# Performance work log

Measured on AMD Instinct MI355X. Metric: run time of the kernel, lower is better.

The kernel has to match this reference:

```python
import jax, jax.numpy as jnp
import numpy as np

K = 1024
H = 16
HEAD = K // H

def setup_inputs() -> dict:
    key = jax.random.key(0)
    ks = jax.random.split(key, 6)
    b, t = 2, 2048
    x = jax.random.normal(ks[0], (b, t, K), dtype=jnp.float32)
    padding = jnp.ones((b, t), dtype=jnp.int32)
    s = 1.0 / np.sqrt(K)
    Wq = jax.random.normal(ks[1], (K, K), dtype=jnp.float32) * s
    Wk = jax.random.normal(ks[2], (K, K), dtype=jnp.float32) * s
    Wv = jax.random.normal(ks[3], (K, K), dtype=jnp.float32) * s
    Wo = jax.random.normal(ks[4], (K, K), dtype=jnp.float32) * s
    bo = jnp.zeros((K,), dtype=jnp.float32)
    return {"x": x, "padding": padding, "Wq": Wq, "Wk": Wk, "Wv": Wv, "Wo": Wo, "bo": bo}

def reference(x, padding, Wq, Wk, Wv, Wo, bo):
    b, t, k = x.shape
    h, d = H, HEAD
    # projections (nn.Linear: x @ W.T), then split heads -> [b,h,t,d]
    q = (x @ Wq.T).reshape(b, t, h, d).transpose(0, 2, 1, 3)
    kk = (x @ Wk.T).reshape(b, t, h, d).transpose(0, 2, 1, 3)
    v = (x @ Wv.T).reshape(b, t, h, d).transpose(0, 2, 1, 3)
    scores = jnp.einsum('bhqd,bhkd->bhqk', q, kk)
    # key-side padding mask: positions with padding==0 get -inf (before scaling,
    # same result since -inf/sqrt(d) == -inf)
    mask = (padding == 0)[:, None, None, :]  # [b,1,1,t]
    scores = jnp.where(mask, -jnp.inf, scores) / np.sqrt(d).astype(np.float32)
    weights = jax.nn.softmax(scores, axis=-1)
    out = jnp.einsum('bhqk,bhkd->bhqd', weights, v)
    out = out.transpose(0, 2, 1, 3).reshape(b, t, h * d)
    return out @ Wo.T + bo
```

## Files before the change

### kernel.cpp

```cpp
#include <hip/hip_runtime.h>
#include <hip/hip_bf16.h>
#include <cmath>
#include <stdint.h>

#define K_DIM 1024
#define NH    16
#define HD    64
#define T     2048
#define NTOK  4096
#define NBH   32

typedef __bf16 bf16x8 __attribute__((ext_vector_type(8)));
typedef float  f32x4  __attribute__((ext_vector_type(4)));
typedef float  f32x16 __attribute__((ext_vector_type(16)));

__device__ __forceinline__ unsigned short f2bf(float f) {
  union { float f; unsigned u; } v; v.f = f;
  unsigned u = v.u;
  return (unsigned short)((u + 0x7FFFu + ((u >> 16) & 1u)) >> 16);
}
__device__ __forceinline__ ushort4 pk4(float a, float b, float c, float d) {
  union { __hip_bfloat162 h[2]; ushort4 u; } r;
  r.h[0] = __float22bfloat162_rn(float2{a, b});
  r.h[1] = __float22bfloat162_rn(float2{c, d});
  return r.u;
}
__device__ __forceinline__ int pk2(float a, float b) {
  union { __hip_bfloat162 h; int u; } r;
  r.h = __float22bfloat162_rn(float2{a, b});
  return r.u;
}

__device__ __forceinline__ void gload16(const void* g, void* l) {
  __builtin_amdgcn_global_load_lds(
      (__attribute__((address_space(1))) void*)(g),
      (__attribute__((address_space(3))) void*)(l),
      16, 0, 0);
}

__global__ void convert_kernel(const float* __restrict__ x,
                               const float* __restrict__ Wq,
                               const float* __restrict__ Wk,
                               const float* __restrict__ Wv,
                               const float* __restrict__ Wo,
                               unsigned short* __restrict__ xb,
                               unsigned short* __restrict__ wqkv,
                               unsigned short* __restrict__ wob)
{
  const size_t NX = (size_t)NTOK * K_DIM;
  const size_t NW = (size_t)K_DIM * K_DIM;
  size_t i = ((size_t)blockIdx.x * blockDim.x + threadIdx.x) * 4;
  const float* src; unsigned short* dst; size_t off;
  float scale = 1.f;
  if (i < NX)             { src = x;  dst = xb;          off = i; }
  else if (i < NX + NW)   { src = Wq; dst = wqkv;        off = i - NX;
                            scale = 0.18033688011112042f; }
  else if (i < NX + 2*NW) { src = Wk; dst = wqkv + NW;   off = i - NX - NW; }
  else if (i < NX + 3*NW) { src = Wv; dst = wqkv + 2*NW; off = i - NX - 2*NW; }
  else                    { src = Wo; dst = wob;         off = i - NX - 3*NW; }
  float4 v = *(const float4*)(src + off);
  *(ushort4*)(dst + off) = pk4(v.x * scale, v.y * scale, v.z * scale, v.w * scale);
}

template <int MODE, int TM, int TN>
__global__ __launch_bounds__(256, 2)
void gemm_bt(const unsigned short* __restrict__ A,
             const unsigned short* __restrict__ B,
             unsigned short* __restrict__ o_q,
             unsigned short* __restrict__ o_k,
             unsigned short* __restrict__ o_v,
             float* __restrict__ o_f,
             const float* __restrict__ bias)
{
  __shared__ unsigned short Asm[TM * 64];
  __shared__ unsigned short Bsm[TN * 64];
  const int tid  = threadIdx.x;
  const int wave = tid >> 6;
  const int lane = tid & 63;
  const int lq   = lane & 15;
  const int quad = lane >> 4;
  const int bm = blockIdx.x, bn = blockIdx.y;
  const int wm = (wave >> 1) * (TM / 2), wn = (wave & 1) * (TN / 2);
  const int MT = TM / 32, NT = TN / 32;

  f32x4 acc[MT][NT];
#pragma unroll
  for (int i = 0; i < MT; ++i)
#pragma unroll
    for (int j = 0; j < NT; ++j) acc[i][j] = (f32x4){0.f, 0.f, 0.f, 0.f};

  const char* Ab = (const char*)(A + (size_t)bm * TM * K_DIM);
  const char* Bb = (const char*)(B + (size_t)bn * TN * K_DIM);

  for (int k0 = 0; k0 < K_DIM; k0 += 64) {
#pragma unroll
    for (int i = 0; i < MT; ++i) {
      int off   = i * 4096 + wave * 1024 + lane * 16;
      int row   = off >> 7;
      int chunk = (off >> 4) & 7;
      int scol  = (chunk ^ (row & 7)) << 4;
      gload16(Ab + (size_t)row * (K_DIM * 2) + (size_t)k0 * 2 + scol,
              (char*)Asm + off - lane * 16);
    }
#pragma unroll
    for (int i = 0; i < NT; ++i) {
      int off   = i * 4096 + wave * 1024 + lane * 16;
      int row   = off >> 7;
      int chunk = (off >> 4) & 7;
      int scol  = (chunk ^ (row & 7)) << 4;
      gload16(Bb + (size_t)row * (K_DIM * 2) + (size_t)k0 * 2 + scol,
              (char*)Bsm + off - lane * 16);
    }
    __syncthreads();
#pragma unroll
    for (int kk = 0; kk < 64; kk += 32) {
      bf16x8 af[MT], bfr[NT];
#pragma unroll
      for (int mt = 0; mt < MT; ++mt) {
        int row = wm + mt * 16 + lq;
        int sw  = (quad + (kk >> 3)) ^ (row & 7);
        af[mt] = *(const bf16x8*)((const char*)Asm + row * 128 + (sw << 4));
      }
#pragma unroll
      for (int nt = 0; nt < NT; ++nt) {
        int row = wn + nt * 16 + lq;
        int sw  = (quad + (kk >> 3)) ^ (row & 7);
        bfr[nt] = *(const bf16x8*)((const char*)Bsm + row * 128 + (sw << 4));
      }
#pragma unroll
      for (int mt = 0; mt < MT; ++mt)
#pragma unroll
        for (int nt = 0; nt < NT; ++nt)
          acc[mt][nt] = __builtin_amdgcn_mfma_f32_16x16x32_bf16(af[mt], bfr[nt], acc[mt][nt], 0, 0, 0);
    }
    __syncthreads();
  }

#pragma unroll
  for (int mt = 0; mt < MT; ++mt) {
    int mbase = bm * TM + wm + mt * 16 + quad * 4;
#pragma unroll
    for (int nt = 0; nt < NT; ++nt) {
      int n = bn * TN + wn + nt * 16 + lq;
      if (MODE == 1) {
        int which = mbase >> 10, c = mbase & 1023;
        int h = c >> 6, d0 = c & 63;
        int b = n >> 11, t = n & 2047;
        if (which < 2) {
          ushort4 pk = pk4(acc[mt][nt][0], acc[mt][nt][1], acc[mt][nt][2], acc[mt][nt][3]);
          unsigned short* dst = which ? o_k : o_q;
          *(ushort4*)&dst[((size_t)(b * NH + h) * T + t) * HD + d0] = pk;
        } else {
#pragma unroll
          for (int r = 0; r < 4; ++r)
            o_v[((size_t)(b * NH + h) * HD + d0 + r) * T + t] = f2bf(acc[mt][nt][r]);
        }
      } else {
        float4 bv = *(const float4*)&bias[mbase];
        float4 o;
        o.x = acc[mt][nt][0] + bv.x; o.y = acc[mt][nt][1] + bv.y;
        o.z = acc[mt][nt][2] + bv.z; o.w = acc[mt][nt][3] + bv.w;
        *(float4*)&o_f[(size_t)n * K_DIM + mbase] = o;
      }
    }
  }
}

__global__ __launch_bounds__(256, 2)
void attn_kernel(const unsigned short* __restrict__ Q,
                 const unsigned short* __restrict__ Kb,
                 const unsigned short* __restrict__ Vt,
                 const int* __restrict__ padding,
                 unsigned short* __restrict__ O)
{
  __shared__ unsigned short Ksm[128 * 64];
  __shared__ unsigned short Vsm[2][64 * 128];
  __shared__ float Lsm[4][32];

  const int tid  = threadIdx.x;
  const int wave = tid >> 6;
  const int lane = tid & 63;
  const int l31  = lane & 31;
  const int hw   = lane >> 5;
  const int bh = blockIdx.x;
  const int qt = blockIdx.y;
  const int b  = bh >> 4;
  const int h  = bh & 15;
  const int qbase = qt * 128 + wave * 32;

  bf16x8 qf[4];
#pragma unroll
  for (int kk = 0; kk < 4; ++kk)
    qf[kk] = *(const bf16x8*)&Q[((size_t)bh * T + qbase + l31) * HD + kk * 16 + hw * 8];

  f32x16 o_acc[2];
#pragma unroll
  for (int db = 0; db < 2; ++db)
#pragma unroll
    for (int r = 0; r < 16; ++r) o_acc[db][r] = 0.f;
  float l_part = 0.f;

  auto stage = [&](int kt, int buf) {
#pragma unroll
    for (int i = 0; i < 4; ++i) {
      int off = i * 4096 + wave * 1024 + lane * 16;
      {
        int row = off >> 7, chunk = (off >> 4) & 7;
        int scol = (chunk ^ (row & 7)) << 4;
        gload16((const char*)Kb + ((size_t)(bh * T + kt * 128 + row) * HD) * 2 + scol,
                (char*)Ksm + off - lane * 16);
      }
      {
        int row = off >> 8, chunk = (off >> 4) & 15;
        int scol = (chunk ^ (row & 15)) << 4;
        gload16((const char*)Vt + ((size_t)(bh * HD + row) * T + (size_t)kt * 128) * 2 + scol,
                (char*)Vsm[buf] + off - lane * 16);
      }
    }
  };

  stage(0, 0);
  __syncthreads();

  for (int kt = 0; kt < T / 128; ++kt) {
    const int cur = kt & 1;

    f32x16 st[4];
#pragma unroll
    for (int nt = 0; nt < 4; ++nt)
#pragma unroll
      for (int r = 0; r < 16; ++r) st[nt][r] = 0.f;
#pragma unroll
    for (int kk = 0; kk < 4; ++kk) {
#pragma unroll
      for (int nt = 0; nt < 4; ++nt) {
        int row = nt * 32 + l31;
        int sw  = (2 * kk + hw) ^ (row & 7);
        bf16x8 kf = *(const bf16x8*)((const char*)Ksm + row * 128 + (sw << 4));
        st[nt] = __builtin_amdgcn_mfma_f32_32x32x16_bf16(kf, qf[kk], st[nt], 0, 0, 0);
      }
    }

    __syncthreads();

    if (kt < T / 128 - 1) stage(kt + 1, cur ^ 1);

#pragma unroll
    for (int nt = 0; nt < 4; ++nt) {
      int dw[8];
#pragma unroll
      for (int g = 0; g < 4; ++g) {
        int4 pd = *(const int4*)&padding[b * T + kt * 128 + nt * 32 + g * 8 + hw * 4];
        float p0 = pd.x ? __builtin_amdgcn_exp2f(st[nt][g * 4 + 0]) : 0.f;
        float p1 = pd.y ? __builtin_amdgcn_exp2f(st[nt][g * 4 + 1]) : 0.f;
        float p2 = pd.z ? __builtin_amdgcn_exp2f(st[nt][g * 4 + 2]) : 0.f;
        float p3 = pd.w ? __builtin_amdgcn_exp2f(st[nt][g * 4 + 3]) : 0.f;
        l_part += (p0 + p1) + (p2 + p3);
        dw[g * 2]     = pk2(p0, p1);
        dw[g * 2 + 1] = pk2(p2, p3);
      }
      union PA { int d[4]; bf16x8 v; } pa0, pa1;
      {
        int a0 = dw[0], c0 = dw[2];
        int a1 = dw[1], c1 = dw[3];
        asm("v_permlane32_swap_b32 %0, %1" : "+v"(a0), "+v"(c0));
        asm("v_permlane32_swap_b32 %0, %1" : "+v"(a1), "+v"(c1));
        pa0.d[0] = a0; pa0.d[1] = a1; pa0.d[2] = c0; pa0.d[3] = c1;
        int b0 = dw[4], d0 = dw[6];
        int b1 = dw[5], d1 = dw[7];
        asm("v_permlane32_swap_b32 %0, %1" : "+v"(b0), "+v"(d0));
        asm("v_permlane32_swap_b32 %0, %1" : "+v"(b1), "+v"(d1));
        pa1.d[0] = b0; pa1.d[1] = b1; pa1.d[2] = d0; pa1.d[3] = d1;
      }
#pragma unroll
      for (int j = 0; j < 2; ++j) {
        bf16x8 pav = j ? pa1.v : pa0.v;
#pragma unroll
        for (int db = 0; db < 2; ++db) {
          int row = db * 32 + l31;
          int g2  = 4 * nt + 2 * j + hw;
          int sw  = g2 ^ (row & 15);
          bf16x8 vf = *(const bf16x8*)((const char*)Vsm[cur] + row * 256 + (sw << 4));
          o_acc[db] = __builtin_amdgcn_mfma_f32_32x32x16_bf16(pav, vf, o_acc[db], 0, 0, 0);
        }
      }
    }

    __syncthreads();
  }

  float lsum = l_part + __shfl_xor(l_part, 32);
  float inv  = (lsum > 0.f) ? 1.f / lsum : 0.f;
  Lsm[wave][l31] = inv;
  __syncthreads();
  f32x4 inv4[4];
#pragma unroll
  for (int g = 0; g < 4; ++g)
    inv4[g] = *(const f32x4*)&Lsm[wave][g * 8 + hw * 4];
#pragma unroll
  for (int db = 0; db < 2; ++db) {
#pragma unroll
    for (int r = 0; r < 16; ++r) {
      int qrow = (r & 3) + 8 * (r >> 2) + 4 * hw;
      int t    = qbase + qrow;
      int chan = h * HD + db * 32 + l31;
      O[((size_t)(b * T + t)) * K_DIM + chan] = f2bf(o_acc[db][r] * inv4[r >> 2][r & 3]);
    }
  }
}

extern "C" void kernel_launch(void* const* d_in, const int* in_sizes, int n_in,
                              void* d_out, int out_size, void* d_ws, size_t ws_size,
                              hipStream_t stream)
{
  const float* x       = (const float*)d_in[0];
  const int*   padding = (const int*)d_in[1];
  const float* Wq      = (const float*)d_in[2];
  const float* Wk      = (const float*)d_in[3];
  const float* Wv      = (const float*)d_in[4];
  const float* Wo      = (const float*)d_in[5];
  const float* bo      = (const float*)d_in[6];
  float* out = (float*)d_out;

  char* ws = (char*)d_ws;
  unsigned short* xb   = (unsigned short*)(ws);
  unsigned short* wqkv = (unsigned short*)(ws + (8u  << 20));
  unsigned short* wob  = (unsigned short*)(ws + (14u << 20));
  unsigned short* qb   = (unsigned short*)(ws + (16u << 20));
  unsigned short* kb   = (unsigned short*)(ws + (24u << 20));
  unsigned short* vtb  = (unsigned short*)(ws + (32u << 20));
  unsigned short* ab   = (unsigned short*)(ws + (40u << 20));

  convert_kernel<<<8192, 256, 0, stream>>>(x, Wq, Wk, Wv, Wo, xb, wqkv, wob);

  gemm_bt<1, 192, 128><<<dim3(16, 32), 256, 0, stream>>>(wqkv, xb, qb, kb, vtb, nullptr, nullptr);

  attn_kernel<<<dim3(32, 16), 256, 0, stream>>>(qb, kb, vtb, padding, ab);

  gemm_bt<2, 64, 128><<<dim3(16, 32), 256, 0, stream>>>(wob, ab, nullptr, nullptr, nullptr, out, bo);
}
```

Before: 205.0 us.

## Double-buffer K tiles, prefetch early, interleave QK^T with softmax per tile

K shared-memory staging becomes double-buffered, so the next tile's K and V loads are issued at the start of each iteration rather than after the QK^T pass and a mid-loop barrier. The score computation is restructured to run one 32-key subtile at a time, feeding its exp/PV work directly. This lowers live score registers from four accumulators to one and removes a __syncthreads. The K swizzle also changes to a row-dependent XOR pattern to cut LDS bank conflicts, at the cost of more LDS use, which may affect occupancy at 2 blocks per CU.

```diff
diff --git a/kernel.cpp b/kernel.cpp
--- a/kernel.cpp
+++ b/kernel.cpp
@@ -173,7 +173,7 @@
                  const int* __restrict__ padding,
                  unsigned short* __restrict__ O)
 {
-  __shared__ unsigned short Ksm[128 * 64];
+  __shared__ unsigned short Ksm[2][128 * 64];
   __shared__ unsigned short Vsm[2][64 * 128];
   __shared__ float Lsm[4][32];
 
@@ -187,6 +187,7 @@
   const int b  = bh >> 4;
   const int h  = bh & 15;
   const int qbase = qt * 128 + wave * 32;
+  const int fk   = (l31 & 7) ^ ((l31 >> 3) & 3);
 
   bf16x8 qf[4];
 #pragma unroll
@@ -206,9 +207,10 @@
       int off = i * 4096 + wave * 1024 + lane * 16;
       {
         int row = off >> 7, chunk = (off >> 4) & 7;
-        int scol = (chunk ^ (row & 7)) << 4;
+        int f   = (row & 7) ^ ((row >> 3) & 3);
+        int scol = (chunk ^ f) << 4;
         gload16((const char*)Kb + ((size_t)(bh * T + kt * 128 + row) * HD) * 2 + scol,
-                (char*)Ksm + off - lane * 16);
+                (char*)Ksm[buf] + off - lane * 16);
       }
       {
         int row = off >> 8, chunk = (off >> 4) & 15;
@@ -225,36 +227,29 @@
   for (int kt = 0; kt < T / 128; ++kt) {
     const int cur = kt & 1;
 
-    f32x16 st[4];
-#pragma unroll
-    for (int nt = 0; nt < 4; ++nt)
-#pragma unroll
-      for (int r = 0; r < 16; ++r) st[nt][r] = 0.f;
-#pragma unroll
-    for (int kk = 0; kk < 4; ++kk) {
-#pragma unroll
-      for (int nt = 0; nt < 4; ++nt) {
+    if (kt < T / 128 - 1) stage(kt + 1, cur ^ 1);
+
+#pragma unroll
+    for (int nt = 0; nt < 4; ++nt) {
+      f32x16 st;
+#pragma unroll
+      for (int r = 0; r < 16; ++r) st[r] = 0.f;
+#pragma unroll
+      for (int kk = 0; kk < 4; ++kk) {
         int row = nt * 32 + l31;
-        int sw  = (2 * kk + hw) ^ (row & 7);
-        bf16x8 kf = *(const bf16x8*)((const char*)Ksm + row * 128 + (sw << 4));
-        st[nt] = __builtin_amdgcn_mfma_f32_32x32x16_bf16(kf, qf[kk], st[nt], 0, 0, 0);
-      }
-    }
-
-    __syncthreads();
-
-    if (kt < T / 128 - 1) stage(kt + 1, cur ^ 1);
-
-#pragma unroll
-    for (int nt = 0; nt < 4; ++nt) {
+        int sw  = (2 * kk + hw) ^ fk;
+        bf16x8 kf = *(const bf16x8*)((const char*)Ksm[cur] + row * 128 + (sw << 4));
+        st = __builtin_amdgcn_mfma_f32_32x32x16_bf16(kf, qf[kk], st, 0, 0, 0);
+      }
+
       int dw[8];
 #pragma unroll
       for (int g = 0; g < 4; ++g) {
         int4 pd = *(const int4*)&padding[b * T + kt * 128 + nt * 32 + g * 8 + hw * 4];
-        float p0 = pd.x ? __builtin_amdgcn_exp2f(st[nt][g * 4 + 0]) : 0.f;
-        float p1 = pd.y ? __builtin_amdgcn_exp2f(st[nt][g * 4 + 1]) : 0.f;
-        float p2 = pd.z ? __builtin_amdgcn_exp2f(st[nt][g * 4 + 2]) : 0.f;
-        float p3 = pd.w ? __builtin_amdgcn_exp2f(st[nt][g * 4 + 3]) : 0.f;
+        float p0 = pd.x ? __builtin_amdgcn_exp2f(st[g * 4 + 0]) : 0.f;
+        float p1 = pd.y ? __builtin_amdgcn_exp2f(st[g * 4 + 1]) : 0.f;
+        float p2 = pd.z ? __builtin_amdgcn_exp2f(st[g * 4 + 2]) : 0.f;
+        float p3 = pd.w ? __builtin_amdgcn_exp2f(st[g * 4 + 3]) : 0.f;
         l_part += (p0 + p1) + (p2 + p3);
         dw[g * 2]     = pk2(p0, p1);
         dw[g * 2 + 1] = pk2(p2, p3);
```

New measurement: 189.5 us. 1.08x faster.

## Double-buffer K tiles, drop mid-loop barrier, split PV accumulators

Applied to the files above, without the earlier changes.

K shared memory becomes double-buffered, so the next K/V tile can be prefetched at the top of each iteration and the barrier between QK^T and PV is removed. The K swizzle adds a row>>3 term to reduce LDS bank conflicts, and its XOR index is hoisted out of the inner loop. P fragments are built for all tiles before the PV MFMAs, which accumulate into two independent chains that are summed at the end, along with two partial row sums. This costs more LDS (which may limit occupancy with 2 blocks per CU) and more accumulator registers.

```diff
diff --git a/kernel.cpp b/kernel.cpp
--- a/kernel.cpp
+++ b/kernel.cpp
@@ -173,7 +173,7 @@
                  const int* __restrict__ padding,
                  unsigned short* __restrict__ O)
 {
-  __shared__ unsigned short Ksm[128 * 64];
+  __shared__ unsigned short Ksm[2][128 * 64];
   __shared__ unsigned short Vsm[2][64 * 128];
   __shared__ float Lsm[4][32];
 
@@ -187,18 +187,21 @@
   const int b  = bh >> 4;
   const int h  = bh & 15;
   const int qbase = qt * 128 + wave * 32;
+  const int fk   = (l31 & 7) ^ ((l31 >> 3) & 3);
 
   bf16x8 qf[4];
 #pragma unroll
   for (int kk = 0; kk < 4; ++kk)
     qf[kk] = *(const bf16x8*)&Q[((size_t)bh * T + qbase + l31) * HD + kk * 16 + hw * 8];
 
-  f32x16 o_acc[2];
-#pragma unroll
-  for (int db = 0; db < 2; ++db)
-#pragma unroll
-    for (int r = 0; r < 16; ++r) o_acc[db][r] = 0.f;
-  float l_part = 0.f;
+  f32x16 oj[2][2];
+#pragma unroll
+  for (int j = 0; j < 2; ++j)
+#pragma unroll
+    for (int db = 0; db < 2; ++db)
+#pragma unroll
+      for (int r = 0; r < 16; ++r) oj[j][db][r] = 0.f;
+  float lp0 = 0.f, lp1 = 0.f;
 
   auto stage = [&](int kt, int buf) {
 #pragma unroll
@@ -206,9 +209,10 @@
       int off = i * 4096 + wave * 1024 + lane * 16;
       {
         int row = off >> 7, chunk = (off >> 4) & 7;
-        int scol = (chunk ^ (row & 7)) << 4;
+        int f   = (row & 7) ^ ((row >> 3) & 3);
+        int scol = (chunk ^ f) << 4;
         gload16((const char*)Kb + ((size_t)(bh * T + kt * 128 + row) * HD) * 2 + scol,
-                (char*)Ksm + off - lane * 16);
+                (char*)Ksm[buf] + off - lane * 16);
       }
       {
         int row = off >> 8, chunk = (off >> 4) & 15;
@@ -225,6 +229,8 @@
   for (int kt = 0; kt < T / 128; ++kt) {
     const int cur = kt & 1;
 
+    if (kt < T / 128 - 1) stage(kt + 1, cur ^ 1);
+
     f32x16 st[4];
 #pragma unroll
     for (int nt = 0; nt < 4; ++nt)
@@ -232,19 +238,16 @@
       for (int r = 0; r < 16; ++r) st[nt][r] = 0.f;
 #pragma unroll
     for (int kk = 0; kk < 4; ++kk) {
+      int sw = (2 * kk + hw) ^ fk;
 #pragma unroll
       for (int nt = 0; nt < 4; ++nt) {
         int row = nt * 32 + l31;
-        int sw  = (2 * kk + hw) ^ (row & 7);
-        bf16x8 kf = *(const bf16x8*)((const char*)Ksm + row * 128 + (sw << 4));
+        bf16x8 kf = *(const bf16x8*)((const char*)Ksm[cur] + row * 128 + (sw << 4));
         st[nt] = __builtin_amdgcn_mfma_f32_32x32x16_bf16(kf, qf[kk], st[nt], 0, 0, 0);
       }
     }
 
-    __syncthreads();
-
-    if (kt < T / 128 - 1) stage(kt + 1, cur ^ 1);
-
+    union PA { int d[4]; bf16x8 v; } paA[4], paB[4];
 #pragma unroll
     for (int nt = 0; nt < 4; ++nt) {
       int dw[8];
@@ -255,33 +258,37 @@
         float p1 = pd.y ? __builtin_amdgcn_exp2f(st[nt][g * 4 + 1]) : 0.f;
         float p2 = pd.z ? __builtin_amdgcn_exp2f(st[nt][g * 4 + 2]) : 0.f;
         float p3 = pd.w ? __builtin_amdgcn_exp2f(st[nt][g * 4 + 3]) : 0.f;
-        l_part += (p0 + p1) + (p2 + p3);
+        if (g & 1) lp1 += (p0 + p1) + (p2 + p3);
+        else       lp0 += (p0 + p1) + (p2 + p3);
         dw[g * 2]     = pk2(p0, p1);
         dw[g * 2 + 1] = pk2(p2, p3);
       }
-      union PA { int d[4]; bf16x8 v; } pa0, pa1;
       {
         int a0 = dw[0], c0 = dw[2];
         int a1 = dw[1], c1 = dw[3];
         asm("v_permlane32_swap_b32 %0, %1" : "+v"(a0), "+v"(c0));
         asm("v_permlane32_swap_b32 %0, %1" : "+v"(a1), "+v"(c1));
-        pa0.d[0] = a0; pa0.d[1] = a1; pa0.d[2] = c0; pa0.d[3] = c1;
+        paA[nt].d[0] = a0; paA[nt].d[1] = a1; paA[nt].d[2] = c0; paA[nt].d[3] = c1;
         int b0 = dw[4], d0 = dw[6];
         int b1 = dw[5], d1 = dw[7];
         asm("v_permlane32_swap_b32 %0, %1" : "+v"(b0), "+v"(d0));
         asm("v_permlane32_swap_b32 %0, %1" : "+v"(b1), "+v"(d1));
-        pa1.d[0] = b0; pa1.d[1] = b1; pa1.d[2] = d0; pa1.d[3] = d1;
-      }
+        paB[nt].d[0] = b0; paB[nt].d[1] = b1; paB[nt].d[2] = d0; paB[nt].d[3] = d1;
+      }
+    }
+
+#pragma unroll
+    for (int nt = 0; nt < 4; ++nt) {
 #pragma unroll
       for (int j = 0; j < 2; ++j) {
-        bf16x8 pav = j ? pa1.v : pa0.v;
+        bf16x8 pav = j ? paB[nt].v : paA[nt].v;
 #pragma unroll
         for (int db = 0; db < 2; ++db) {
           int row = db * 32 + l31;
           int g2  = 4 * nt + 2 * j + hw;
           int sw  = g2 ^ (row & 15);
           bf16x8 vf = *(const bf16x8*)((const char*)Vsm[cur] + row * 256 + (sw << 4));
-          o_acc[db] = __builtin_amdgcn_mfma_f32_32x32x16_bf16(pav, vf, o_acc[db], 0, 0, 0);
+          oj[j][db] = __builtin_amdgcn_mfma_f32_32x32x16_bf16(pav, vf, oj[j][db], 0, 0, 0);
         }
       }
     }
@@ -289,7 +296,8 @@
     __syncthreads();
   }
 
-  float lsum = l_part + __shfl_xor(l_part, 32);
+  float lsum = (lp0 + lp1);
+  lsum += __shfl_xor(lsum, 32);
   float inv  = (lsum > 0.f) ? 1.f / lsum : 0.f;
   Lsm[wave][l31] = inv;
   __syncthreads();
@@ -304,7 +312,8 @@
       int qrow = (r & 3) + 8 * (r >> 2) + 4 * hw;
       int t    = qbase + qrow;
       int chan = h * HD + db * 32 + l31;
-      O[((size_t)(b * T + t)) * K_DIM + chan] = f2bf(o_acc[db][r] * inv4[r >> 2][r & 3]);
+      float ov = oj[0][db][r] + oj[1][db][r];
+      O[((size_t)(b * T + t)) * K_DIM + chan] = f2bf(ov * inv4[r >> 2][r & 3]);
     }
   }
 }
```

Result: faster. 188.4 us (-8.1%).
